# Optimization experiments

Measured on AMD Instinct MI355X. Metric: run time of the kernel, lower is better.

## Reference

```python
import jax, jax.numpy as jnp
import numpy as np

EMBED_DIM = 4096
NUM_HEADS = 32
NUM_KV_HEADS = 8
HEAD_DIM = EMBED_DIM // NUM_HEADS          # 128
Q_PER_KV = NUM_HEADS // NUM_KV_HEADS       # 4
KV_DIM = HEAD_DIM * NUM_KV_HEADS           # 1024
ROPE_BASE = 10000.0
ROTARY_DIM = HEAD_DIM                      # rotary_emb_dim = 128 (full head)


def setup_inputs() -> dict:
    key = jax.random.key(0)
    k1, k2, k3 = jax.random.split(key, 3)
    b, s = 2, 2048
    x = jax.random.normal(k1, (b, s, EMBED_DIM), dtype=jnp.float32)
    # torch nn.Linear weight layout: (out_features, in_features); scaled init
    wqkv_w = jax.random.normal(k2, (EMBED_DIM + 2 * KV_DIM, EMBED_DIM), dtype=jnp.float32) * (EMBED_DIM ** -0.5)
    wo_w = jax.random.normal(k3, (EMBED_DIM, EMBED_DIM), dtype=jnp.float32) * (EMBED_DIM ** -0.5)
    return {"x": x, "wqkv_w": wqkv_w, "wo_w": wo_w}


def _rope_cos_sin(seqlen, dtype):
    inv_freq = 1.0 / (ROPE_BASE ** (jnp.arange(0, ROTARY_DIM, 2, dtype=jnp.float32) / ROTARY_DIM))
    t = jnp.arange(seqlen, dtype=jnp.float32)
    freqs = jnp.outer(t, inv_freq)                 # (s, d/2)
    emb = jnp.concatenate([freqs, freqs], axis=-1)  # (s, d) — HF convention
    return jnp.cos(emb).astype(dtype), jnp.sin(emb).astype(dtype)


def _rotate_half(x):
    x1, x2 = jnp.split(x, 2, axis=-1)
    return jnp.concatenate([-x2, x1], axis=-1)


def _apply_rope(x, cos, sin):
    # x: (b, s, h, d); cos/sin: (s, d)
    c = cos[None, :, None, :]
    s_ = sin[None, :, None, :]
    return x * c + _rotate_half(x) * s_


def reference(x, wqkv_w, wo_w):
    b, s, _ = x.shape
    # packed QKV projection
    qkv = jnp.einsum("bse,fe->bsf", x, wqkv_w)
    # b s (h_kv * (q_per_kv + 2) * d) -> b s h_kv (q_per_kv+2) d
    qkv = qkv.reshape(b, s, NUM_KV_HEADS, Q_PER_KV + 2, HEAD_DIM)
    q = qkv[..., :Q_PER_KV, :].reshape(b, s, NUM_HEADS, HEAD_DIM)
    k = qkv[..., -2, :]   # (b, s, h_kv, d)
    v = qkv[..., -1, :]   # (b, s, h_kv, d)

    # RoPE (HF rotate_half impl, offsets = 0)
    cos, sin = _rope_cos_sin(s, x.dtype)
    q = _apply_rope(q, cos, sin)
    k = _apply_rope(k, cos, sin)

    # GQA: expand kv heads to match q heads
    k = jnp.repeat(k, Q_PER_KV, axis=2)   # (b, s, h, d)
    v = jnp.repeat(v, Q_PER_KV, axis=2)

    scale = HEAD_DIM ** -0.5
    scores = jnp.einsum("bqhd,bkhd->bhqk", q, k) * scale
    causal_mask = jnp.tril(jnp.ones((s, s), dtype=bool))
    scores = jnp.where(causal_mask[None, None], scores, jnp.finfo(scores.dtype).min)
    probs = jax.nn.softmax(scores, axis=-1)
    context = jnp.einsum("bhqk,bkhd->bqhd", probs, v)
    context = context.reshape(b, s, EMBED_DIM)
    return jnp.einsum("bse,fe->bsf", context, wo_w)
```

## Files before the change

kernel.cpp:

```cpp
#include <hip/hip_runtime.h>
#include <hip/hip_bf16.h>
#include <stdint.h>

typedef __hip_bfloat16 bf16;
typedef short bf16x8 __attribute__((ext_vector_type(8)));
typedef float f32x4 __attribute__((ext_vector_type(4)));

#define MFMA16(a, b, c) __builtin_amdgcn_mfma_f32_16x16x32_bf16((a), (b), (c), 0, 0, 0)

__device__ __forceinline__ void gload16(const void* g, void* l) {
  __builtin_amdgcn_global_load_lds((const __attribute__((address_space(1))) void*)g,
                                   (__attribute__((address_space(3))) void*)l,
                                   16, 0, 0);
}

__device__ __forceinline__ void stv(float* p, float v) { *p = v; }
__device__ __forceinline__ void stv(bf16* p, float v) { *p = __float2bfloat16(v); }

__device__ __forceinline__ float row_max16(float v) {
  int t = __builtin_amdgcn_update_dpp(0, __float_as_int(v), 0xB1, 0xF, 0xF, true);
  v = fmaxf(v, __int_as_float(t));
  t = __builtin_amdgcn_update_dpp(0, __float_as_int(v), 0x4E, 0xF, 0xF, true);
  v = fmaxf(v, __int_as_float(t));
  t = __builtin_amdgcn_update_dpp(0, __float_as_int(v), 0x124, 0xF, 0xF, true);
  v = fmaxf(v, __int_as_float(t));
  t = __builtin_amdgcn_update_dpp(0, __float_as_int(v), 0x128, 0xF, 0xF, true);
  v = fmaxf(v, __int_as_float(t));
  return v;
}
__device__ __forceinline__ float row_sum16(float v) {
  int t = __builtin_amdgcn_update_dpp(0, __float_as_int(v), 0xB1, 0xF, 0xF, true);
  v += __int_as_float(t);
  t = __builtin_amdgcn_update_dpp(0, __float_as_int(v), 0x4E, 0xF, 0xF, true);
  v += __int_as_float(t);
  t = __builtin_amdgcn_update_dpp(0, __float_as_int(v), 0x124, 0xF, 0xF, true);
  v += __int_as_float(t);
  t = __builtin_amdgcn_update_dpp(0, __float_as_int(v), 0x128, 0xF, 0xF, true);
  v += __int_as_float(t);
  return v;
}

__global__ void cast_f32_bf16(const float* __restrict__ in, bf16* __restrict__ out,
                              long n) {
  const long stride = (long)gridDim.x * blockDim.x * 8;
  for (long i = ((long)blockIdx.x * blockDim.x + threadIdx.x) * 8; i < n; i += stride) {
    const float4 a = *(const float4*)&in[i];
    const float4 b = *(const float4*)&in[i + 4];
    bf16 t[8];
    t[0] = __float2bfloat16(a.x); t[1] = __float2bfloat16(a.y);
    t[2] = __float2bfloat16(a.z); t[3] = __float2bfloat16(a.w);
    t[4] = __float2bfloat16(b.x); t[5] = __float2bfloat16(b.y);
    t[6] = __float2bfloat16(b.z); t[7] = __float2bfloat16(b.w);
    *(bf16x8*)&out[i] = *(const bf16x8*)t;
  }
}

template <typename OutT>
__global__ __launch_bounds__(512, 2) void gemm256(const bf16* __restrict__ A,
                                                  const bf16* __restrict__ B,
                                                  OutT* __restrict__ C,
                                                  int M, int N, int K) {
  const int nbn = N >> 8;
  const int nwg = gridDim.x;
  const int wg = blockIdx.x;
  const int cpx = nwg >> 3;
  const int swz = (wg & 7) * cpx + (wg >> 3);
  const int bm = swz / nbn;
  const int bn = swz - bm * nbn;

  __shared__ bf16 As[2][256][64];
  __shared__ bf16 Bs[2][256][64];

  const int tid = threadIdx.x;
  const int wave = tid >> 6, lane = tid & 63;
  const int lo = lane & 15, hi = lane >> 4;
  const int wm = wave >> 2, wn = wave & 3;

  const bf16* Ag = A + (long)(bm * 256) * K;
  const bf16* Bg = B + (long)(bn * 256) * K;

  int srow[2], scol[2], sdst[2];
#pragma unroll
  for (int j = 0; j < 2; j++) {
    const int c = j * 512 + tid;
    const int row = c >> 3;
    srow[j] = row;
    scol[j] = ((c & 7) ^ (row & 7)) * 8;
    sdst[j] = (j * 512 + wave * 64) * 8;
  }

#define STG(G, S, kt, h)                                                      \
  {                                                                           \
    _Pragma("unroll") for (int j = 0; j < 2; j++)                             \
        gload16((G) + (long)((h)*128 + srow[j]) * K + (kt) + scol[j],         \
                (S) + (h)*8192 + sdst[j]);                                    \
  }

  f32x4 acc[8][4] = {};
  const int NT = K >> 6;

  STG(Ag, &As[0][0][0], 0, 0); STG(Ag, &As[0][0][0], 0, 1);
  STG(Bg, &Bs[0][0][0], 0, 0); STG(Bg, &Bs[0][0][0], 0, 1);
  STG(Ag, &As[1][0][0], 64, 0); STG(Ag, &As[1][0][0], 64, 1);

#pragma unroll 1
  for (int t = 0; t < NT; ++t) {
    if (t >= NT - 1) asm volatile("s_waitcnt vmcnt(0)" ::: "memory");
    else             asm volatile("s_waitcnt vmcnt(4)" ::: "memory");
    __builtin_amdgcn_s_barrier();

    const bf16* Ab = &As[t & 1][0][0];
    const bf16* Bb = &Bs[t & 1][0][0];
    bf16* SAn = &As[t & 1][0][0];
    bf16* SBn = &Bs[(t + 1) & 1][0][0];
    const int kt1 = (t + 1) * 64, kt2 = (t + 2) * 64;
    const bool s1 = (t + 1 < NT), s2 = (t + 2 < NT);
    const int c0 = (hi ^ (lo & 7)) * 8;
    const int c1 = ((4 + hi) ^ (lo & 7)) * 8;

    bf16x8 a0[4], a1[4], a2[4], a3[4], b0[4], b1[4];

#pragma unroll
    for (int m = 0; m < 4; m++) {
      const int row = (wm * 128 + m * 16 + lo) * 64;
      a0[m] = *(const bf16x8*)&Ab[row + c0];
      a1[m] = *(const bf16x8*)&Ab[row + c1];
    }
#pragma unroll
    for (int n = 0; n < 4; n++)
      b0[n] = *(const bf16x8*)&Bb[(wn * 64 + n * 16 + lo) * 64 + c0];
    if (s1) STG(Bg, SBn, kt1, 0);
    __builtin_amdgcn_s_barrier();
    asm volatile("s_waitcnt lgkmcnt(0)" ::: "memory");
    __builtin_amdgcn_sched_barrier(0);
    __builtin_amdgcn_s_setprio(1);
#pragma unroll
    for (int m = 0; m < 4; m++)
#pragma unroll
      for (int n = 0; n < 4; n++) acc[m][n] = MFMA16(a0[m], b0[n], acc[m][n]);
    __builtin_amdgcn_s_setprio(0);
    __builtin_amdgcn_s_barrier();

#pragma unroll
    for (int m = 0; m < 4; m++) {
      const int row = (wm * 128 + 64 + m * 16 + lo) * 64;
      a2[m] = *(const bf16x8*)&Ab[row + c0];
      a3[m] = *(const bf16x8*)&Ab[row + c1];
    }
    if (s1) STG(Bg, SBn, kt1, 1);
    __builtin_amdgcn_s_barrier();
    asm volatile("s_waitcnt lgkmcnt(0)" ::: "memory");
    __builtin_amdgcn_sched_barrier(0);
    __builtin_amdgcn_s_setprio(1);
#pragma unroll
    for (int m = 0; m < 4; m++)
#pragma unroll
      for (int n = 0; n < 4; n++) acc[4 + m][n] = MFMA16(a2[m], b0[n], acc[4 + m][n]);
    __builtin_amdgcn_s_setprio(0);
    __builtin_amdgcn_s_barrier();

#pragma unroll
    for (int n = 0; n < 4; n++)
      b1[n] = *(const bf16x8*)&Bb[(wn * 64 + n * 16 + lo) * 64 + c1];
    if (s2) STG(Ag, SAn, kt2, 0);
    __builtin_amdgcn_s_barrier();
    asm volatile("s_waitcnt lgkmcnt(0)" ::: "memory");
    __builtin_amdgcn_sched_barrier(0);
    __builtin_amdgcn_s_setprio(1);
#pragma unroll
    for (int m = 0; m < 4; m++)
#pragma unroll
      for (int n = 0; n < 4; n++) acc[m][n] = MFMA16(a1[m], b1[n], acc[m][n]);
    __builtin_amdgcn_s_setprio(0);
    __builtin_amdgcn_s_barrier();

    if (s2) STG(Ag, SAn, kt2, 1);
    __builtin_amdgcn_s_barrier();
    __builtin_amdgcn_s_setprio(1);
#pragma unroll
    for (int m = 0; m < 4; m++)
#pragma unroll
      for (int n = 0; n < 4; n++) acc[4 + m][n] = MFMA16(a3[m], b1[n], acc[4 + m][n]);
    __builtin_amdgcn_s_setprio(0);
  }
#undef STG

  const long crow0 = (long)bm * 256 + wm * 128;
  const long ccol0 = (long)bn * 256 + wn * 64;
#pragma unroll
  for (int m = 0; m < 8; m++)
#pragma unroll
    for (int n = 0; n < 4; n++)
#pragma unroll
      for (int r = 0; r < 4; r++)
        stv(&C[(crow0 + m * 16 + hi * 4 + r) * (long)N + ccol0 + n * 16 + lo],
            acc[m][n][r]);
}

__global__ void rope_qk(bf16* __restrict__ qkv) {
  const int row = blockIdx.x;
  const int t = row & 2047;
  const float scale = 0.08838834764831845f;
  for (int p = threadIdx.x; p < 40 * 64; p += blockDim.x) {
    const int sh = p >> 6, j = p & 63;
    const int kvh = sh / 5, slot = sh - kvh * 5;
    const long base = (long)row * 6144 + kvh * 768 + slot * 128 + j;
    const float x1 = __bfloat162float(qkv[base]);
    const float x2 = __bfloat162float(qkv[base + 64]);
    const float inv = __expf(-(float)j * 0.14391156831212787f);
    const float ang = (float)t * inv;
    const float c = cosf(ang), s = sinf(ang);
    float o1 = x1 * c - x2 * s;
    float o2 = x2 * c + x1 * s;
    if (slot < 4) { o1 *= scale; o2 *= scale; }
    qkv[base] = __float2bfloat16(o1);
    qkv[base + 64] = __float2bfloat16(o2);
  }
}

__global__ void vtrans(const bf16* __restrict__ qkv, bf16* __restrict__ Vt) {
  const int tt = blockIdx.x, dd = blockIdx.y, bk = blockIdx.z;
  const int kvh = bk & 7, b = bk >> 3;
  __shared__ bf16 tile[64][65];
  const int tx = threadIdx.x, ty = threadIdx.y;
  const bf16* src = qkv + ((long)(b * 2048 + tt * 64)) * 6144 + kvh * 768 + 640 + dd * 64;
  for (int r = ty; r < 64; r += 4) tile[r][tx] = src[(long)r * 6144 + tx];
  __syncthreads();
  bf16* dst = Vt + ((long)bk * 128 + dd * 64) * 2048 + tt * 64;
  for (int r = ty; r < 64; r += 4) dst[(long)r * 2048 + tx] = tile[tx][r];
}

__global__ __launch_bounds__(256) void attn(const bf16* __restrict__ qkv,
                                            const bf16* __restrict__ Vt,
                                            bf16* __restrict__ Ctx) {
  const int lin = blockIdx.x;
  const int c = (lin & 7) * 64 + (lin >> 3);
  const int z = c & 31;
  const int kvh = (c >> 5) & 7;
  const int b = c >> 8;

  const int wave = threadIdx.x >> 6;
  const int lane = threadIdx.x & 63;
  const int h = kvh * 4 + wave;
  const int lo = lane & 15, hi = lane >> 4;

  const bf16* Qb = qkv + (long)b * 2048 * 6144 + kvh * 768 + wave * 128;
  const bf16* Kb = qkv + (long)b * 2048 * 6144 + kvh * 768 + 512;
  const bf16* Vb = Vt + ((long)(b * 8 + kvh)) * 128 * 2048;

  __shared__ bf16 Plds[4][32][40];

#pragma unroll 1
  for (int pass = 0; pass < 2; ++pass) {
    const int qw = pass ? 63 - z : z;
    const int q0 = qw * 32;

    bf16x8 qf[2][4];
#pragma unroll
    for (int qb = 0; qb < 2; qb++)
#pragma unroll
      for (int dc = 0; dc < 4; dc++)
        qf[qb][dc] =
            *(const bf16x8*)&Qb[(long)(q0 + qb * 16 + lo) * 6144 + dc * 32 + hi * 8];

    f32x4 acc[2][8] = {};
    float mrow[2][4], lrow[2][4];
#pragma unroll
    for (int qb = 0; qb < 2; qb++)
#pragma unroll
      for (int r = 0; r < 4; r++) {
        mrow[qb][r] = -1e30f;
        lrow[qb][r] = 0.0f;
      }

    for (int kt = 0; kt <= qw; ++kt) {
      const int k0 = kt * 32;
      f32x4 sacc[2][2] = {};
      __builtin_amdgcn_s_setprio(1);
#pragma unroll
      for (int kb = 0; kb < 2; kb++)
#pragma unroll
        for (int dc = 0; dc < 4; dc++) {
          const bf16x8 kf =
              *(const bf16x8*)&Kb[(long)(k0 + kb * 16 + lo) * 6144 + dc * 32 + hi * 8];
          sacc[0][kb] = MFMA16(qf[0][dc], kf, sacc[0][kb]);
          sacc[1][kb] = MFMA16(qf[1][dc], kf, sacc[1][kb]);
        }
      __builtin_amdgcn_s_setprio(0);

      if (kt == qw) {
#pragma unroll
        for (int qb = 0; qb < 2; qb++)
#pragma unroll
          for (int kb = 0; kb < 2; kb++) {
            const int q = q0 + qb * 16 + hi * 4;
            const int k = k0 + kb * 16 + lo;
#pragma unroll
            for (int r = 0; r < 4; r++)
              if (k > q + r) sacc[qb][kb][r] = -1e30f;
          }
      }

      float ex = -1.0f;
#pragma unroll
      for (int qb = 0; qb < 2; qb++)
#pragma unroll
        for (int kb = 0; kb < 2; kb++)
#pragma unroll
          for (int r = 0; r < 4; r++)
            ex = fmaxf(ex, sacc[qb][kb][r] - mrow[qb][r]);

      if (!__all(ex <= 0.0f)) {
        float sf[2][4];
#pragma unroll
        for (int qb = 0; qb < 2; qb++)
#pragma unroll
          for (int r = 0; r < 4; r++) {
            const float pm = row_max16(fmaxf(sacc[qb][0][r], sacc[qb][1][r]));
            const float mn = fmaxf(mrow[qb][r], pm);
            sf[qb][r] = __expf(mrow[qb][r] - mn);
            mrow[qb][r] = mn;
            lrow[qb][r] *= sf[qb][r];
          }
#pragma unroll
        for (int qb = 0; qb < 2; qb++)
#pragma unroll
          for (int dt = 0; dt < 8; dt++)
#pragma unroll
            for (int r = 0; r < 4; r++) acc[qb][dt][r] *= sf[qb][r];
      }

#pragma unroll
      for (int qb = 0; qb < 2; qb++)
#pragma unroll
        for (int r = 0; r < 4; r++) {
          float p0 = __expf(sacc[qb][0][r] - mrow[qb][r]);
          float p1 = __expf(sacc[qb][1][r] - mrow[qb][r]);
          lrow[qb][r] += row_sum16(p0 + p1);
          Plds[wave][qb * 16 + hi * 4 + r][lo] = __float2bfloat16(p0);
          Plds[wave][qb * 16 + hi * 4 + r][16 + lo] = __float2bfloat16(p1);
        }

      bf16x8 pa[2];
#pragma unroll
      for (int qb = 0; qb < 2; qb++)
        pa[qb] = *(const bf16x8*)&Plds[wave][qb * 16 + lo][hi * 8];

      __builtin_amdgcn_s_setprio(1);
#pragma unroll
      for (int dt = 0; dt < 8; dt++) {
        const bf16x8 vf = *(const bf16x8*)&Vb[(long)(dt * 16 + lo) * 2048 + k0 + hi * 8];
        acc[0][dt] = MFMA16(pa[0], vf, acc[0][dt]);
        acc[1][dt] = MFMA16(pa[1], vf, acc[1][dt]);
      }
      __builtin_amdgcn_s_setprio(0);
    }

#pragma unroll
    for (int qb = 0; qb < 2; qb++)
#pragma unroll
      for (int r = 0; r < 4; r++) {
        const float rl = 1.0f / lrow[qb][r];
#pragma unroll
        for (int dt = 0; dt < 8; dt++) {
          const float o = acc[qb][dt][r] * rl;
          const long row = (long)b * 2048 + q0 + qb * 16 + hi * 4 + r;
          Ctx[row * 4096 + h * 128 + dt * 16 + lo] = __float2bfloat16(o);
        }
      }
  }
}


extern "C" void kernel_launch(void* const* d_in, const int* in_sizes, int n_in,
                              void* d_out, int out_size, void* d_ws, size_t ws_size,
                              hipStream_t stream) {
  (void)in_sizes; (void)n_in; (void)out_size; (void)ws_size;
  const float* x = (const float*)d_in[0];
  const float* wqkv = (const float*)d_in[1];
  const float* wo = (const float*)d_in[2];
  float* out = (float*)d_out;

  const long NX = 4096L * 4096;
  const long NW1 = 6144L * 4096;

  const size_t XB_B = (size_t)NX * 2;
  const size_t WQ_B = (size_t)NW1 * 2;
  const size_t QKV_B = WQ_B;

  char* w = (char*)d_ws;
  bf16* xb = (bf16*)w;
  bf16* wqkvb = (bf16*)(w + XB_B);
  bf16* qkvp = (bf16*)(w + XB_B + WQ_B);
  bf16* Vtp = (bf16*)(w + XB_B + WQ_B + QKV_B);
  bf16* wob = xb;
  bf16* ctx = wqkvb;

  cast_f32_bf16<<<2048, 256, 0, stream>>>(x, xb, NX);
  cast_f32_bf16<<<2048, 256, 0, stream>>>(wqkv, wqkvb, NW1);

  gemm256<bf16><<<16 * 24, 512, 0, stream>>>(xb, wqkvb, qkvp, 4096, 6144, 4096);

  rope_qk<<<4096, 256, 0, stream>>>(qkvp);
  vtrans<<<dim3(32, 2, 16), dim3(64, 4), 0, stream>>>(qkvp, Vtp);

  cast_f32_bf16<<<2048, 256, 0, stream>>>(wo, wob, NX);

  attn<<<dim3(512), 256, 0, stream>>>(qkvp, Vtp, ctx);

  gemm256<float><<<16 * 16, 512, 0, stream>>>(ctx, wob, out, 4096, 4096, 4096);
}
```

Measured before the change: 664.9 us.

## Stage K/V tiles into double-buffered swizzled LDS via async global-to-LDS loads

The attention kernel now loads each 32-key K tile and V^T tile cooperatively into LDS using global_load_lds, double-buffered so the next-but-one tile is prefetched while the current one is consumed. Before, all four waves read the same K/V data directly from global memory. The LDS layout uses an XOR swizzle to avoid bank conflicts on the MFMA fragment reads. In exchange it adds two barriers per iteration, explicit vmcnt waits and more LDS use, which could lower occupancy.

After: 645.4 us. 1.03x faster.

```diff
diff --git a/kernel.cpp b/kernel.cpp
--- a/kernel.cpp
+++ b/kernel.cpp
@@ -239,8 +239,9 @@
   const int kvh = (c >> 5) & 7;
   const int b = c >> 8;
 
-  const int wave = threadIdx.x >> 6;
-  const int lane = threadIdx.x & 63;
+  const int tid = threadIdx.x;
+  const int wave = tid >> 6;
+  const int lane = tid & 63;
   const int h = kvh * 4 + wave;
   const int lo = lane & 15, hi = lane >> 4;
 
@@ -248,7 +249,30 @@
   const bf16* Kb = qkv + (long)b * 2048 * 6144 + kvh * 768 + 512;
   const bf16* Vb = Vt + ((long)(b * 8 + kvh)) * 128 * 2048;
 
+  __shared__ bf16 Kl[2][32][128];
+  __shared__ bf16 Vl[2][128][32];
   __shared__ bf16 Plds[4][32][40];
+
+  int krow[2], kcol[2], vrow[2], vcol[2], sbase[2];
+#pragma unroll
+  for (int cl = 0; cl < 2; cl++) {
+    const int t = cl * 256 + tid;
+    krow[cl] = t >> 4;
+    kcol[cl] = ((t & 15) ^ (krow[cl] & 15)) * 8;
+    vrow[cl] = t >> 2;
+    vcol[cl] = ((t & 3) ^ ((vrow[cl] >> 1) & 3)) * 8;
+    sbase[cl] = cl * 2048 + wave * 512;
+  }
+
+#define STAGE_KV(bufi, k0_)                                                    \
+  {                                                                            \
+    _Pragma("unroll") for (int cl = 0; cl < 2; cl++)                           \
+        gload16(Kb + (long)((k0_) + krow[cl]) * 6144 + kcol[cl],               \
+                &Kl[bufi][0][0] + sbase[cl]);                                  \
+    _Pragma("unroll") for (int cl = 0; cl < 2; cl++)                           \
+        gload16(Vb + (long)vrow[cl] * 2048 + (k0_) + vcol[cl],                 \
+                &Vl[bufi][0][0] + sbase[cl]);                                  \
+  }
 
 #pragma unroll 1
   for (int pass = 0; pass < 2; ++pass) {
@@ -273,16 +297,27 @@
         lrow[qb][r] = 0.0f;
       }
 
+    STAGE_KV(0, 0);
+    if (qw > 0) STAGE_KV(1, 32);
+
+#pragma unroll 1
     for (int kt = 0; kt <= qw; ++kt) {
+      if (kt < qw) asm volatile("s_waitcnt vmcnt(4)" ::: "memory");
+      else         asm volatile("s_waitcnt vmcnt(0)" ::: "memory");
+      __builtin_amdgcn_s_barrier();
+
+      const int bi = kt & 1;
       const int k0 = kt * 32;
+
       f32x4 sacc[2][2] = {};
       __builtin_amdgcn_s_setprio(1);
 #pragma unroll
       for (int kb = 0; kb < 2; kb++)
 #pragma unroll
         for (int dc = 0; dc < 4; dc++) {
-          const bf16x8 kf =
-              *(const bf16x8*)&Kb[(long)(k0 + kb * 16 + lo) * 6144 + dc * 32 + hi * 8];
+          const int row = kb * 16 + lo;
+          const int p = (dc * 4 + hi) ^ (row & 15);
+          const bf16x8 kf = *(const bf16x8*)&Kl[bi][row][p * 8];
           sacc[0][kb] = MFMA16(qf[0][dc], kf, sacc[0][kb]);
           sacc[1][kb] = MFMA16(qf[1][dc], kf, sacc[1][kb]);
         }
@@ -349,11 +384,17 @@
       __builtin_amdgcn_s_setprio(1);
 #pragma unroll
       for (int dt = 0; dt < 8; dt++) {
-        const bf16x8 vf = *(const bf16x8*)&Vb[(long)(dt * 16 + lo) * 2048 + k0 + hi * 8];
+        const int row = dt * 16 + lo;
+        const int p = hi ^ ((row >> 1) & 3);
+        const bf16x8 vf = *(const bf16x8*)&Vl[bi][row][p * 8];
         acc[0][dt] = MFMA16(pa[0], vf, acc[0][dt]);
         acc[1][dt] = MFMA16(pa[1], vf, acc[1][dt]);
       }
       __builtin_amdgcn_s_setprio(0);
+
+      asm volatile("s_waitcnt lgkmcnt(0)" ::: "memory");
+      __builtin_amdgcn_s_barrier();
+      if (kt + 2 <= qw) STAGE_KV(bi, (kt + 2) * 32);
     }
 
 #pragma unroll
@@ -369,6 +410,7 @@
         }
       }
   }
+#undef STAGE_KV
 }
 
 
```
